# Optimization experiments

Measured on AMD Instinct MI355X. Metric: run time of the kernel, lower is better.

Reference implementation:

```python
import jax, jax.numpy as jnp
import numpy as np

B, Hs, Ws, C = 1, 48, 48, 768
NH = 12
HD = C // NH          # 64
L = Hs * Ws           # 2304
THETA = 10000.0
SCALE = HD ** -0.5
EPS = 1e-5

# relative coord index table: rel_idx[i, j] = i - j + (H - 1), as in _setup_rel_pos
_REL_IDX = jnp.asarray(np.arange(Hs)[:, None] - np.arange(Ws)[None, :] + (Hs - 1))


def _rope_cos_sin():
    """2D axial RoPE angles (compute_axial_cis): [L, HD//2] cos/sin tables."""
    nf = HD // 4
    freqs = 1.0 / (THETA ** (np.arange(0, HD, 4)[:nf].astype(np.float32) / HD))
    t = np.arange(L, dtype=np.float32)
    tx = t % Hs               # x coord cycles fastest (init_t_xy)
    ty = np.floor(t / Hs)
    ang = np.concatenate([np.outer(tx, freqs), np.outer(ty, freqs)], axis=-1)  # [L, HD//2]
    return jnp.asarray(np.cos(ang)), jnp.asarray(np.sin(ang))


def _layernorm(x, w, b):
    mu = x.mean(-1, keepdims=True)
    var = ((x - mu) ** 2).mean(-1, keepdims=True)
    return (x - mu) * jax.lax.rsqrt(var + EPS) * w + b


def _apply_rope(t, cos, sin):
    # t: [B, NH, L, HD]; view as complex pairs (even=real, odd=imag)
    tr = t.reshape(*t.shape[:-1], HD // 2, 2)
    re, im = tr[..., 0], tr[..., 1]
    out = jnp.stack([re * cos - im * sin, re * sin + im * cos], axis=-1)
    return out.reshape(t.shape)


def setup_inputs() -> dict:
    key = jax.random.key(0)
    ks = jax.random.split(key, 8)
    def rn(k, shape, std=0.02):
        return jax.random.normal(k, shape, dtype=jnp.float32) * std
    return {
        "x": jax.random.normal(ks[0], (B, Hs, Ws, C), dtype=jnp.float32),
        "ln1_w": jnp.ones((C,), jnp.float32),
        "ln1_b": jnp.zeros((C,), jnp.float32),
        "qkv_w": rn(ks[1], (3 * C, C)),
        "qkv_b": jnp.zeros((3 * C,), jnp.float32),
        "rel_pos_h": rn(ks[2], (2 * Hs - 1, HD)),
        "rel_pos_w": rn(ks[3], (2 * Ws - 1, HD)),
        "proj_w": rn(ks[4], (C, C)),
        "proj_b": jnp.zeros((C,), jnp.float32),
        "ln2_w": jnp.ones((C,), jnp.float32),
        "ln2_b": jnp.zeros((C,), jnp.float32),
        "fc1_w": rn(ks[5], (4 * C, C)),
        "fc1_b": jnp.zeros((4 * C,), jnp.float32),
        "fc2_w": rn(ks[6], (C, 4 * C)),
        "fc2_b": jnp.zeros((C,), jnp.float32),
    }


def reference(x, ln1_w, ln1_b, qkv_w, qkv_b, rel_pos_h, rel_pos_w, proj_w, proj_b,
              ln2_w, ln2_b, fc1_w, fc1_b, fc2_w, fc2_b):
    shortcut = x
    h = _layernorm(x, ln1_w, ln1_b)                         # [B,H,W,C]
    qkv = h.reshape(B, L, C) @ qkv_w.T + qkv_b              # [B,L,3C]
    qkv = qkv.reshape(B, L, 3, NH, HD).transpose(2, 0, 3, 1, 4)
    q, k, v = qkv[0], qkv[1], qkv[2]                        # [B,NH,L,HD]

    cos, sin = _rope_cos_sin()
    cos, sin = cos[None, None], sin[None, None]
    q = _apply_rope(q, cos, sin)
    k = _apply_rope(k, cos, sin)

    # Decomposed relative-position bias; math-equivalent to concat_rel_pos
    # (q' = [q*rescale, gathered-rel-vecs], k' = [k, one-hots]) followed by SDPA.
    rq = q.reshape(B, NH, Hs, Ws, HD)
    Rh = rel_pos_h[_REL_IDX]                                # [Hs, Hs(kh), HD]
    Rw = rel_pos_w[_REL_IDX]                                # [Ws, Ws(kw), HD]
    bias_h = jnp.einsum('bnhwc,hkc->bnhwk', rq, Rh)         # over key-row
    bias_w = jnp.einsum('bnhwc,wkc->bnhwk', rq, Rw)         # over key-col

    scores = jnp.einsum('bnqc,bnkc->bnqk', q, k) * SCALE    # [B,NH,L,L]
    scores = scores.reshape(B, NH, Hs, Ws, Hs, Ws) + bias_h[..., :, None] + bias_w[..., None, :]
    attn = jax.nn.softmax(scores.reshape(B, NH, L, L), axis=-1)
    out = jnp.einsum('bnqk,bnkc->bnqc', attn, v)            # [B,NH,L,HD]
    out = out.transpose(0, 2, 1, 3).reshape(B, L, C) @ proj_w.T + proj_b

    x = shortcut + out.reshape(B, Hs, Ws, C)
    h = _layernorm(x, ln2_w, ln2_b)
    h = jax.nn.gelu(h @ fc1_w.T + fc1_b, approximate=False)
    x = x + (h @ fc2_w.T + fc2_b)
    return x
```

## Files before the change

### kernel.cpp

```cpp
#include <hip/hip_runtime.h>
#include <math.h>

#define LTOK 2304
#define CDIM 768
#define NHEAD 12
#define HDIM 64
#define HS 48

typedef short s16x8 __attribute__((ext_vector_type(8)));
typedef float f32x4 __attribute__((ext_vector_type(4)));

__device__ __forceinline__ unsigned short f2b(float f) {
  __bf16 b = (__bf16)f;
  return __builtin_bit_cast(unsigned short, b);
}
__device__ __forceinline__ float b2f(unsigned short u) {
  unsigned int x = ((unsigned int)u) << 16;
  return __builtin_bit_cast(float, x);
}

__device__ __forceinline__ void gld_lds16(void* lds, const void* g) {
  __builtin_amdgcn_global_load_lds(
      (const __attribute__((address_space(1))) unsigned int*)g,
      (__attribute__((address_space(3))) unsigned int*)lds, 16, 0, 0);
}

__global__ __launch_bounds__(256) void f2b_kernel(const float* __restrict__ in,
                                                  unsigned short* __restrict__ out, int n) {
  const int i = (blockIdx.x * 256 + threadIdx.x) * 8;
  if (i + 8 > n) return;
  float4 v0 = *(const float4*)(in + i);
  float4 v1 = *(const float4*)(in + i + 4);
  alignas(16) unsigned short o[8] = {f2b(v0.x), f2b(v0.y), f2b(v0.z), f2b(v0.w),
                                     f2b(v1.x), f2b(v1.y), f2b(v1.z), f2b(v1.w)};
  *(uint4*)(out + i) = *(const uint4*)o;
}

__global__ __launch_bounds__(256) void ln_kernel(const float* __restrict__ x,
                                                 const float* __restrict__ w,
                                                 const float* __restrict__ b,
                                                 unsigned short* __restrict__ out) {
  const int row = blockIdx.x;
  const int t = threadIdx.x;
  const float* xr = x + (size_t)row * CDIM;
  float v0 = xr[t], v1 = xr[t + 256], v2 = xr[t + 512];
  float s = v0 + v1 + v2;
  float ss = v0 * v0 + v1 * v1 + v2 * v2;
#pragma unroll
  for (int off = 32; off > 0; off >>= 1) {
    s += __shfl_down(s, off, 64);
    ss += __shfl_down(ss, off, 64);
  }
  __shared__ float rs[4], rss[4];
  if ((t & 63) == 0) { rs[t >> 6] = s; rss[t >> 6] = ss; }
  __syncthreads();
  float S = rs[0] + rs[1] + rs[2] + rs[3];
  float SS = rss[0] + rss[1] + rss[2] + rss[3];
  const float inv_c = 1.0f / (float)CDIM;
  float mu = S * inv_c;
  float var = SS * inv_c - mu * mu;
  float inv = rsqrtf(var + 1e-5f);
  unsigned short* orow = out + (size_t)row * CDIM;
  orow[t]       = f2b((v0 - mu) * inv * w[t]       + b[t]);
  orow[t + 256] = f2b((v1 - mu) * inv * w[t + 256] + b[t + 256]);
  orow[t + 512] = f2b((v2 - mu) * inv * w[t + 512] + b[t + 512]);
}

template <bool GELU, bool RES, bool OUTBF>
__global__ __launch_bounds__(256) void mfma_gemm(const unsigned short* __restrict__ A,
                                                 const unsigned short* __restrict__ B,
                                                 const float* __restrict__ bias,
                                                 const float* __restrict__ res,
                                                 void* __restrict__ Cout,
                                                 int M, int N, int K) {
  __shared__ unsigned short As[128 * 32];
  __shared__ unsigned short Bs[128 * 32];
  const int t = threadIdx.x;
  const int lane = t & 63;
  const int w = t >> 6;
  const int wm = w >> 1, wn = w & 1;
  const int bm = blockIdx.y * 128, bn = blockIdx.x * 128;

  f32x4 acc[4][4] = {};

  const int c0 = 2 * w, c1 = 2 * w + 1;
  const int srow = lane >> 2;
  const int skof = (lane & 3) * 8;
  const unsigned short* Abase = A + (size_t)bm * K + skof;
  const unsigned short* Bbase = B + (size_t)bn * K + skof;
  const int lr = lane & 15, lk = (lane >> 4) * 8, lg = lane >> 4;

  for (int k0 = 0; k0 < K; k0 += 32) {
    gld_lds16(As + c0 * 512, Abase + (size_t)(c0 * 16 + srow) * K + k0);
    gld_lds16(As + c1 * 512, Abase + (size_t)(c1 * 16 + srow) * K + k0);
    gld_lds16(Bs + c0 * 512, Bbase + (size_t)(c0 * 16 + srow) * K + k0);
    gld_lds16(Bs + c1 * 512, Bbase + (size_t)(c1 * 16 + srow) * K + k0);
    __syncthreads();
    s16x8 a[4], b[4];
#pragma unroll
    for (int m = 0; m < 4; ++m)
      a[m] = *(const s16x8*)&As[(wm * 64 + m * 16 + lr) * 32 + lk];
#pragma unroll
    for (int n = 0; n < 4; ++n)
      b[n] = *(const s16x8*)&Bs[(wn * 64 + n * 16 + lr) * 32 + lk];
#pragma unroll
    for (int m = 0; m < 4; ++m)
#pragma unroll
      for (int n = 0; n < 4; ++n)
        acc[m][n] = __builtin_amdgcn_mfma_f32_16x16x32_bf16(a[m], b[n], acc[m][n], 0, 0, 0);
    __syncthreads();
  }

#pragma unroll
  for (int n = 0; n < 4; ++n) {
    const int col = bn + wn * 64 + n * 16 + lr;
    const float bc = bias[col];
#pragma unroll
    for (int m = 0; m < 4; ++m) {
#pragma unroll
      for (int j = 0; j < 4; ++j) {
        const int row = bm + wm * 64 + m * 16 + lg * 4 + j;
        float v = acc[m][n][j] + bc;
        if (GELU) v = 0.5f * v * (1.0f + erff(v * 0.70710678118654752f));
        if (RES) v += res[(size_t)row * N + col];
        if (OUTBF) ((unsigned short*)Cout)[(size_t)row * N + col] = f2b(v);
        else       ((float*)Cout)[(size_t)row * N + col] = v;
      }
    }
  }
}

__global__ __launch_bounds__(256) void rope_cs_kernel(float* __restrict__ cs,
                                                      float* __restrict__ sn) {
  const int idx = blockIdx.x * 256 + threadIdx.x;
  const int l = idx >> 5;
  const int i = idx & 31;
  const int j = i & 15;
  const float f = __expf(-(float)j * 0.57564627324851142f);
  const float coord = (i < 16) ? (float)(l % HS) : (float)(l / HS);
  const float ang = coord * f;
  cs[idx] = cosf(ang);
  sn[idx] = sinf(ang);
}

__global__ __launch_bounds__(256) void prep_kernel(const float* __restrict__ qkv,
                                                   const float* __restrict__ cs,
                                                   const float* __restrict__ sn,
                                                   unsigned short* __restrict__ Qb,
                                                   unsigned short* __restrict__ Kb,
                                                   unsigned short* __restrict__ Vb) {
  __shared__ unsigned short Vs[64 * 72];
  const int t = threadIdx.x;
  const int l0 = blockIdx.x * 64, n = blockIdx.y;
  const int r = t >> 2, c = t & 3;
  const int l = l0 + r;
  const float* base = qkv + (size_t)l * (3 * CDIM) + n * HDIM + c * 16;
#pragma unroll
  for (int pq = 0; pq < 2; ++pq) {
    const float* src = base + pq * CDIM;
    const float qs = pq ? 1.0f : 0.125f;
    alignas(16) unsigned short o[16];
#pragma unroll
    for (int i = 0; i < 4; ++i) {
      float4 v = *(const float4*)(src + i * 4);
      const int pr = c * 8 + i * 2;
      const float c0 = cs[l * 32 + pr],     s0 = sn[l * 32 + pr];
      const float c1 = cs[l * 32 + pr + 1], s1 = sn[l * 32 + pr + 1];
      o[i * 4 + 0] = f2b((v.x * c0 - v.y * s0) * qs);
      o[i * 4 + 1] = f2b((v.x * s0 + v.y * c0) * qs);
      o[i * 4 + 2] = f2b((v.z * c1 - v.w * s1) * qs);
      o[i * 4 + 3] = f2b((v.z * s1 + v.w * c1) * qs);
    }
    unsigned short* dst = (pq ? Kb : Qb) + ((size_t)n * LTOK + l) * HDIM + c * 16;
    *(uint4*)dst = *(const uint4*)o;
    *(uint4*)(dst + 8) = *(const uint4*)(o + 8);
  }
  {
    const float* vsrc = base + 2 * CDIM;
    alignas(16) unsigned short vo[16];
#pragma unroll
    for (int i = 0; i < 4; ++i) {
      float4 v = *(const float4*)(vsrc + i * 4);
      vo[i * 4 + 0] = f2b(v.x); vo[i * 4 + 1] = f2b(v.y);
      vo[i * 4 + 2] = f2b(v.z); vo[i * 4 + 3] = f2b(v.w);
    }
    *(uint4*)&Vs[r * 72 + c * 16] = *(const uint4*)vo;
    *(uint4*)&Vs[r * 72 + c * 16 + 8] = *(const uint4*)(vo + 8);
  }
  __syncthreads();
  {
    const int d = t >> 2, kc16 = (t & 3) * 16;
    alignas(16) unsigned short o[16];
#pragma unroll
    for (int i = 0; i < 16; ++i) o[i] = Vs[(kc16 + i) * 72 + d];
    const int kb = (l0 + kc16) >> 3;
    unsigned short* dst0 = Vb + ((size_t)(n * (LTOK / 8) + kb) * 64 + d) * 8;
    unsigned short* dst1 = Vb + ((size_t)(n * (LTOK / 8) + kb + 1) * 64 + d) * 8;
    *(uint4*)dst0 = *(const uint4*)o;
    *(uint4*)dst1 = *(const uint4*)(o + 8);
  }
}

__global__ __launch_bounds__(256) void attn_mfma(const unsigned short* __restrict__ Qb,
                                                 const unsigned short* __restrict__ Kb,
                                                 const unsigned short* __restrict__ Vb,
                                                 const float* __restrict__ relh,
                                                 const float* __restrict__ relw,
                                                 unsigned short* __restrict__ out) {
  __shared__ __align__(16) unsigned char smem[74752];
  unsigned short* const K_lds = (unsigned short*)(smem);
  unsigned short* const V_lds = (unsigned short*)(smem + 24576);
  unsigned short* const P_lds = (unsigned short*)(smem + 53248);
  float* const bh_t = (float*)(smem + 62464);
  unsigned short* const Q_s = (unsigned short*)(smem + 53248);

  const int t = threadIdx.x;
  const int lane = t & 63, w = t >> 6;
  const int p = lane & 15, g = lane >> 4;
  const int l0 = blockIdx.x * 64, n = blockIdx.y;

  const unsigned short* Khead = Kb + (size_t)n * LTOK * HDIM;
  const unsigned short* Vhead = Vb + (size_t)n * (LTOK / 8) * 64 * 8;

  {
    const int r = t >> 2, c = t & 3;
    const unsigned short* src = Qb + ((size_t)n * LTOK + l0 + r) * HDIM + c * 16;
    uint4 v0 = *(const uint4*)src;
    uint4 v1 = *(const uint4*)(src + 8);
    *(uint4*)&Q_s[r * 72 + c * 16] = v0;
    *(uint4*)&Q_s[r * 72 + c * 16 + 8] = v1;
  }
  __syncthreads();

  const int rowb = lane >> 3;
  const int srcc = (lane & 7) ^ rowb;
  const int kc0 = w, kc1 = w + 4, kc2 = w + 8;

  {
    gld_lds16(K_lds + kc0 * 512, Khead + (size_t)(kc0 * 8 + rowb) * HDIM + srcc * 8);
    gld_lds16(K_lds + kc1 * 512, Khead + (size_t)(kc1 * 8 + rowb) * HDIM + srcc * 8);
    gld_lds16(K_lds + kc2 * 512, Khead + (size_t)(kc2 * 8 + rowb) * HDIM + srcc * 8);
    gld_lds16(V_lds + kc0 * 512, Vhead + kc0 * 512 + lane * 8);
    gld_lds16(V_lds + kc1 * 512, Vhead + kc1 * 512 + lane * 8);
    gld_lds16(V_lds + kc2 * 512, Vhead + kc2 * 512 + lane * 8);
  }
  if (t < 128) *(uint4*)&V_lds[6144 + t * 8] = uint4{0u, 0u, 0u, 0u};
  else         *(uint4*)&V_lds[7168 + 6144 + (t - 128) * 8] = uint4{0u, 0u, 0u, 0u};

  const s16x8 qf0 = *(const s16x8*)&Q_s[(w * 16 + p) * 72 + g * 8];
  const s16x8 qf1 = *(const s16x8*)&Q_s[(w * 16 + p) * 72 + 32 + g * 8];

  const int qh_lane = (l0 + lane) / 48;
#pragma unroll
  for (int i = 0; i < 12; ++i) {
    const int kh = w + 4 * i;
    const float* rrow = relh + (size_t)(qh_lane - kh + 47) * HDIM;
    float acc = 0.f;
#pragma unroll
    for (int c8 = 0; c8 < 8; ++c8) {
      s16x8 qv = *(const s16x8*)&Q_s[lane * 72 + c8 * 8];
      float4 ra = *(const float4*)&rrow[c8 * 8];
      float4 rb = *(const float4*)&rrow[c8 * 8 + 4];
      acc += b2f((unsigned short)qv[0]) * ra.x + b2f((unsigned short)qv[1]) * ra.y +
             b2f((unsigned short)qv[2]) * ra.z + b2f((unsigned short)qv[3]) * ra.w +
             b2f((unsigned short)qv[4]) * rb.x + b2f((unsigned short)qv[5]) * rb.y +
             b2f((unsigned short)qv[6]) * rb.z + b2f((unsigned short)qv[7]) * rb.w;
    }
    bh_t[kh * 64 + lane] = acc * 8.0f;
  }

  float bwreg[12];
  {
    const int qrow = w * 16 + p;
    const int qw_lane = (l0 + qrow) % 48;
#pragma unroll
    for (int mb = 0; mb < 3; ++mb)
#pragma unroll
      for (int jj = 0; jj < 4; ++jj) {
        const int j = 16 * mb + 4 * g + jj;
        const float* rrow = relw + (size_t)(qw_lane - j + 47) * HDIM;
        float acc = 0.f;
#pragma unroll
        for (int c8 = 0; c8 < 8; ++c8) {
          s16x8 qv = *(const s16x8*)&Q_s[qrow * 72 + c8 * 8];
          float4 ra = *(const float4*)&rrow[c8 * 8];
          float4 rb = *(const float4*)&rrow[c8 * 8 + 4];
          acc += b2f((unsigned short)qv[0]) * ra.x + b2f((unsigned short)qv[1]) * ra.y +
                 b2f((unsigned short)qv[2]) * ra.z + b2f((unsigned short)qv[3]) * ra.w +
                 b2f((unsigned short)qv[4]) * rb.x + b2f((unsigned short)qv[5]) * rb.y +
                 b2f((unsigned short)qv[6]) * rb.z + b2f((unsigned short)qv[7]) * rb.w;
        }
        bwreg[mb * 4 + jj] = acc * 8.0f;
      }
  }
  __syncthreads();

  {
    uint2 z = {0u, 0u};
    *(uint2*)&P_lds[(w * 16 + p) * 72 + 48 + 4 * g] = z;
  }

  float lsum = 0.f;
  f32x4 accO[4] = {};
  const int sw0 = g ^ (p & 7);
  const int sw1 = (g + 4) ^ (p & 7);
  unsigned short* const Pw = P_lds + w * 16 * 72;

#pragma unroll 1
  for (int kt = 0; kt < 24; ++kt) {
    const int ko = (kt & 1) * 6144;
    const int vo = (kt & 1) * 7168;
    if (kt < 23) {
      const int nko = 6144 - ko, nvo = 7168 - vo;
      const int kb = (kt + 1) * 96;
      const int vb = (kt + 1) * 12;
      gld_lds16(K_lds + nko + kc0 * 512, Khead + (size_t)(kb + kc0 * 8 + rowb) * HDIM + srcc * 8);
      gld_lds16(K_lds + nko + kc1 * 512, Khead + (size_t)(kb + kc1 * 8 + rowb) * HDIM + srcc * 8);
      gld_lds16(K_lds + nko + kc2 * 512, Khead + (size_t)(kb + kc2 * 8 + rowb) * HDIM + srcc * 8);
      gld_lds16(V_lds + nvo + kc0 * 512, Vhead + (vb + kc0) * 512 + lane * 8);
      gld_lds16(V_lds + nvo + kc1 * 512, Vhead + (vb + kc1) * 512 + lane * 8);
      gld_lds16(V_lds + nvo + kc2 * 512, Vhead + (vb + kc2) * 512 + lane * 8);
    }

#pragma unroll 1
    for (int h = 0; h < 2; ++h) {
      f32x4 st[3] = {};
      __builtin_amdgcn_s_setprio(1);
#pragma unroll
      for (int mb = 0; mb < 3; ++mb) {
        const int krow = ko + (h * 48 + 16 * mb + p) * 64;
        s16x8 kf0 = *(const s16x8*)&K_lds[krow + sw0 * 8];
        s16x8 kf1 = *(const s16x8*)&K_lds[krow + sw1 * 8];
        st[mb] = __builtin_amdgcn_mfma_f32_16x16x32_bf16(kf0, qf0, st[mb], 0, 0, 0);
        st[mb] = __builtin_amdgcn_mfma_f32_16x16x32_bf16(kf1, qf1, st[mb], 0, 0, 0);
      }
      __builtin_amdgcn_s_setprio(0);

      const float bhv = bh_t[(2 * kt + h) * 64 + w * 16 + p] - 8.0f;
      float pv[12], ps = 0.f;
#pragma unroll
      for (int mb = 0; mb < 3; ++mb)
#pragma unroll
        for (int jj = 0; jj < 4; ++jj) {
          const float sv = st[mb][jj] + bhv + bwreg[mb * 4 + jj];
          pv[mb * 4 + jj] = __expf(sv);
          ps += pv[mb * 4 + jj];
        }
      lsum += ps;

#pragma unroll
      for (int mb = 0; mb < 3; ++mb) {
        unsigned int lo = (unsigned int)f2b(pv[mb * 4 + 0]) | ((unsigned int)f2b(pv[mb * 4 + 1]) << 16);
        unsigned int hi = (unsigned int)f2b(pv[mb * 4 + 2]) | ((unsigned int)f2b(pv[mb * 4 + 3]) << 16);
        uint2 val = {lo, hi};
        *(uint2*)&Pw[p * 72 + 16 * mb + 4 * g] = val;
      }

      const s16x8 pf0 = *(const s16x8*)&Pw[p * 72 + g * 8];
      const s16x8 pf1 = *(const s16x8*)&Pw[p * 72 + 32 + g * 8];
      __builtin_amdgcn_s_setprio(1);
#pragma unroll
      for (int db = 0; db < 4; ++db) {
        const int drow = 16 * db + p;
        s16x8 vf0 = *(const s16x8*)&V_lds[vo + ((6 * h + g) * 64 + drow) * 8];
        s16x8 vf1 = *(const s16x8*)&V_lds[vo + ((6 * h + 4 + g) * 64 + drow) * 8];
        accO[db] = __builtin_amdgcn_mfma_f32_16x16x32_bf16(vf0, pf0, accO[db], 0, 0, 0);
        accO[db] = __builtin_amdgcn_mfma_f32_16x16x32_bf16(vf1, pf1, accO[db], 0, 0, 0);
      }
      __builtin_amdgcn_s_setprio(0);
    }

    __syncthreads();
  }

  float ls = lsum + __shfl_xor(lsum, 16, 64);
  ls += __shfl_xor(ls, 32, 64);
  const float inv = 1.0f / ls;
  unsigned short* orow = out + (size_t)(l0 + w * 16 + p) * CDIM + n * HDIM;
#pragma unroll
  for (int db = 0; db < 4; ++db) {
    unsigned int lo = (unsigned int)f2b(accO[db][0] * inv) | ((unsigned int)f2b(accO[db][1] * inv) << 16);
    unsigned int hi = (unsigned int)f2b(accO[db][2] * inv) | ((unsigned int)f2b(accO[db][3] * inv) << 16);
    uint2 val = {lo, hi};
    *(uint2*)&orow[16 * db + 4 * g] = val;
  }
}

extern "C" void kernel_launch(void* const* d_in, const int* in_sizes, int n_in,
                              void* d_out, int out_size, void* d_ws, size_t ws_size,
                              hipStream_t stream) {
  const float* x     = (const float*)d_in[0];
  const float* ln1w  = (const float*)d_in[1];
  const float* ln1b  = (const float*)d_in[2];
  const float* qkvw  = (const float*)d_in[3];
  const float* qkvb  = (const float*)d_in[4];
  const float* relh  = (const float*)d_in[5];
  const float* relw  = (const float*)d_in[6];
  const float* projw = (const float*)d_in[7];
  const float* projb = (const float*)d_in[8];
  const float* ln2w  = (const float*)d_in[9];
  const float* ln2b  = (const float*)d_in[10];
  const float* fc1w  = (const float*)d_in[11];
  const float* fc1b  = (const float*)d_in[12];
  const float* fc2w  = (const float*)d_in[13];
  const float* fc2b  = (const float*)d_in[14];
  float* out = (float*)d_out;
  float* ws = (float*)d_ws;

  float* qkv = ws;
  float* x1  = qkv + (size_t)LTOK * 3 * CDIM;
  float* cs  = x1 + (size_t)LTOK * CDIM;
  float* sn  = cs + (size_t)LTOK * 32;
  unsigned short* h_bf    = (unsigned short*)(sn + (size_t)LTOK * 32);
  unsigned short* attn_bf = h_bf + (size_t)LTOK * CDIM;
  unsigned short* wq      = attn_bf + (size_t)LTOK * CDIM;
  unsigned short* wproj   = wq + (size_t)3 * CDIM * CDIM;
  unsigned short* wfc1    = wproj + (size_t)CDIM * CDIM;
  unsigned short* wfc2    = wfc1 + (size_t)4 * CDIM * CDIM;
  unsigned short* Qb      = (unsigned short*)x1;
  unsigned short* Kb      = Qb + (size_t)NHEAD * LTOK * HDIM;
  unsigned short* Vb      = wq;
  unsigned short* m1_bf   = (unsigned short*)qkv;

  f2b_kernel<<<(3 * CDIM * CDIM / 8 + 255) / 256, 256, 0, stream>>>(qkvw, wq, 3 * CDIM * CDIM);
  f2b_kernel<<<(CDIM * CDIM / 8 + 255) / 256, 256, 0, stream>>>(projw, wproj, CDIM * CDIM);
  f2b_kernel<<<(4 * CDIM * CDIM / 8 + 255) / 256, 256, 0, stream>>>(fc1w, wfc1, 4 * CDIM * CDIM);
  f2b_kernel<<<(4 * CDIM * CDIM / 8 + 255) / 256, 256, 0, stream>>>(fc2w, wfc2, 4 * CDIM * CDIM);

  ln_kernel<<<LTOK, 256, 0, stream>>>(x, ln1w, ln1b, h_bf);
  mfma_gemm<false, false, false><<<dim3(18, 18), 256, 0, stream>>>(
      h_bf, wq, qkvb, nullptr, qkv, LTOK, 3 * CDIM, CDIM);
  rope_cs_kernel<<<288, 256, 0, stream>>>(cs, sn);
  prep_kernel<<<dim3(36, 12), 256, 0, stream>>>(qkv, cs, sn, Qb, Kb, Vb);
  attn_mfma<<<dim3(36, 12), 256, 0, stream>>>(Qb, Kb, Vb, relh, relw, attn_bf);
  mfma_gemm<false, true, false><<<dim3(6, 18), 256, 0, stream>>>(
      attn_bf, wproj, projb, x, x1, LTOK, CDIM, CDIM);
  ln_kernel<<<LTOK, 256, 0, stream>>>(x1, ln2w, ln2b, h_bf);
  mfma_gemm<true, false, true><<<dim3(24, 18), 256, 0, stream>>>(
      h_bf, wfc1, fc1b, nullptr, m1_bf, LTOK, 4 * CDIM, CDIM);
  mfma_gemm<false, true, false><<<dim3(6, 18), 256, 0, stream>>>(
      m1_bf, wfc2, fc2b, x1, out, LTOK, CDIM, 4 * CDIM);
}
```

Measured before the change: 276.1 us.

## Split attention key tiles across two wave groups with 512-thread blocks

The attention kernel now launches 512 threads per block. The two 48-key halves of each 96-key tile, previously walked in sequence by one wave, go to separate wave groups (h = w>>2). The half-1 waves pass their partial output accumulators and row sums to the half-0 waves through shared memory at the end. The row-bias table is stored as bf16 so the larger LDS footprint still fits. This aims to double the waves resident per CU and hide MFMA and exp latency on a grid of only 432 blocks, at the cost of an extra reduction step, more LDS, and bf16 rounding of the row bias.

```diff
diff --git a/kernel.cpp b/kernel.cpp
--- a/kernel.cpp
+++ b/kernel.cpp
@@ -201,59 +201,63 @@
   }
 }
 
-__global__ __launch_bounds__(256) void attn_mfma(const unsigned short* __restrict__ Qb,
-                                                 const unsigned short* __restrict__ Kb,
-                                                 const unsigned short* __restrict__ Vb,
-                                                 const float* __restrict__ relh,
-                                                 const float* __restrict__ relw,
-                                                 unsigned short* __restrict__ out) {
-  __shared__ __align__(16) unsigned char smem[74752];
+__global__ __launch_bounds__(512, 4) void attn_mfma(const unsigned short* __restrict__ Qb,
+                                                    const unsigned short* __restrict__ Kb,
+                                                    const unsigned short* __restrict__ Vb,
+                                                    const float* __restrict__ relh,
+                                                    const float* __restrict__ relw,
+                                                    unsigned short* __restrict__ out) {
+  __shared__ __align__(16) unsigned char smem[77824];
   unsigned short* const K_lds = (unsigned short*)(smem);
   unsigned short* const V_lds = (unsigned short*)(smem + 24576);
   unsigned short* const P_lds = (unsigned short*)(smem + 53248);
-  float* const bh_t = (float*)(smem + 62464);
+  unsigned short* const bh16 = (unsigned short*)(smem + 71680);
   unsigned short* const Q_s = (unsigned short*)(smem + 53248);
+  float* const acc_sh = (float*)(smem);
+  float* const ls_sh = (float*)(smem + 16384);
 
   const int t = threadIdx.x;
   const int lane = t & 63, w = t >> 6;
+  const int wq = w & 3, h = w >> 2;
   const int p = lane & 15, g = lane >> 4;
+  const int qrow = wq * 16 + p;
   const int l0 = blockIdx.x * 64, n = blockIdx.y;
 
   const unsigned short* Khead = Kb + (size_t)n * LTOK * HDIM;
   const unsigned short* Vhead = Vb + (size_t)n * (LTOK / 8) * 64 * 8;
 
   {
-    const int r = t >> 2, c = t & 3;
-    const unsigned short* src = Qb + ((size_t)n * LTOK + l0 + r) * HDIM + c * 16;
-    uint4 v0 = *(const uint4*)src;
-    uint4 v1 = *(const uint4*)(src + 8);
-    *(uint4*)&Q_s[r * 72 + c * 16] = v0;
-    *(uint4*)&Q_s[r * 72 + c * 16 + 8] = v1;
+    const int r = t >> 3, c8 = (t & 7) * 8;
+    *(uint4*)&Q_s[r * 72 + c8] =
+        *(const uint4*)(Qb + ((size_t)n * LTOK + l0 + r) * HDIM + c8);
   }
   __syncthreads();
 
   const int rowb = lane >> 3;
   const int srcc = (lane & 7) ^ rowb;
-  const int kc0 = w, kc1 = w + 4, kc2 = w + 8;
-
-  {
-    gld_lds16(K_lds + kc0 * 512, Khead + (size_t)(kc0 * 8 + rowb) * HDIM + srcc * 8);
-    gld_lds16(K_lds + kc1 * 512, Khead + (size_t)(kc1 * 8 + rowb) * HDIM + srcc * 8);
-    gld_lds16(K_lds + kc2 * 512, Khead + (size_t)(kc2 * 8 + rowb) * HDIM + srcc * 8);
-    gld_lds16(V_lds + kc0 * 512, Vhead + kc0 * 512 + lane * 8);
-    gld_lds16(V_lds + kc1 * 512, Vhead + kc1 * 512 + lane * 8);
-    gld_lds16(V_lds + kc2 * 512, Vhead + kc2 * 512 + lane * 8);
+  const int kcA = w;
+  const int kcB = 8 + w;
+  const int vcA = w;
+  const int vcB = 8 + (w - 4);
+
+  {
+    gld_lds16(K_lds + kcA * 512, Khead + (size_t)(kcA * 8 + rowb) * HDIM + srcc * 8);
+    if (w < 4)
+      gld_lds16(K_lds + kcB * 512, Khead + (size_t)(kcB * 8 + rowb) * HDIM + srcc * 8);
+    gld_lds16(V_lds + vcA * 512, Vhead + vcA * 512 + lane * 8);
+    if (w >= 4)
+      gld_lds16(V_lds + vcB * 512, Vhead + vcB * 512 + lane * 8);
   }
   if (t < 128) *(uint4*)&V_lds[6144 + t * 8] = uint4{0u, 0u, 0u, 0u};
-  else         *(uint4*)&V_lds[7168 + 6144 + (t - 128) * 8] = uint4{0u, 0u, 0u, 0u};
-
-  const s16x8 qf0 = *(const s16x8*)&Q_s[(w * 16 + p) * 72 + g * 8];
-  const s16x8 qf1 = *(const s16x8*)&Q_s[(w * 16 + p) * 72 + 32 + g * 8];
+  else if (t < 256) *(uint4*)&V_lds[7168 + 6144 + (t - 128) * 8] = uint4{0u, 0u, 0u, 0u};
+
+  const s16x8 qf0 = *(const s16x8*)&Q_s[qrow * 72 + g * 8];
+  const s16x8 qf1 = *(const s16x8*)&Q_s[qrow * 72 + 32 + g * 8];
 
   const int qh_lane = (l0 + lane) / 48;
 #pragma unroll
-  for (int i = 0; i < 12; ++i) {
-    const int kh = w + 4 * i;
+  for (int i = 0; i < 6; ++i) {
+    const int kh = w + 8 * i;
     const float* rrow = relh + (size_t)(qh_lane - kh + 47) * HDIM;
     float acc = 0.f;
 #pragma unroll
@@ -266,12 +270,11 @@
              b2f((unsigned short)qv[4]) * rb.x + b2f((unsigned short)qv[5]) * rb.y +
              b2f((unsigned short)qv[6]) * rb.z + b2f((unsigned short)qv[7]) * rb.w;
     }
-    bh_t[kh * 64 + lane] = acc * 8.0f;
+    bh16[kh * 64 + lane] = f2b(acc * 8.0f);
   }
 
   float bwreg[12];
   {
-    const int qrow = w * 16 + p;
     const int qw_lane = (l0 + qrow) % 48;
 #pragma unroll
     for (int mb = 0; mb < 3; ++mb)
@@ -297,14 +300,14 @@
 
   {
     uint2 z = {0u, 0u};
-    *(uint2*)&P_lds[(w * 16 + p) * 72 + 48 + 4 * g] = z;
+    *(uint2*)&P_lds[w * 1152 + p * 72 + 48 + 4 * g] = z;
   }
 
   float lsum = 0.f;
   f32x4 accO[4] = {};
   const int sw0 = g ^ (p & 7);
   const int sw1 = (g + 4) ^ (p & 7);
-  unsigned short* const Pw = P_lds + w * 16 * 72;
+  unsigned short* const Pw = P_lds + w * 1152;
 
 #pragma unroll 1
   for (int kt = 0; kt < 24; ++kt) {
@@ -314,75 +317,87 @@
       const int nko = 6144 - ko, nvo = 7168 - vo;
       const int kb = (kt + 1) * 96;
       const int vb = (kt + 1) * 12;
-      gld_lds16(K_lds + nko + kc0 * 512, Khead + (size_t)(kb + kc0 * 8 + rowb) * HDIM + srcc * 8);
-      gld_lds16(K_lds + nko + kc1 * 512, Khead + (size_t)(kb + kc1 * 8 + rowb) * HDIM + srcc * 8);
-      gld_lds16(K_lds + nko + kc2 * 512, Khead + (size_t)(kb + kc2 * 8 + rowb) * HDIM + srcc * 8);
-      gld_lds16(V_lds + nvo + kc0 * 512, Vhead + (vb + kc0) * 512 + lane * 8);
-      gld_lds16(V_lds + nvo + kc1 * 512, Vhead + (vb + kc1) * 512 + lane * 8);
-      gld_lds16(V_lds + nvo + kc2 * 512, Vhead + (vb + kc2) * 512 + lane * 8);
-    }
-
-#pragma unroll 1
-    for (int h = 0; h < 2; ++h) {
-      f32x4 st[3] = {};
-      __builtin_amdgcn_s_setprio(1);
-#pragma unroll
-      for (int mb = 0; mb < 3; ++mb) {
-        const int krow = ko + (h * 48 + 16 * mb + p) * 64;
-        s16x8 kf0 = *(const s16x8*)&K_lds[krow + sw0 * 8];
-        s16x8 kf1 = *(const s16x8*)&K_lds[krow + sw1 * 8];
-        st[mb] = __builtin_amdgcn_mfma_f32_16x16x32_bf16(kf0, qf0, st[mb], 0, 0, 0);
-        st[mb] = __builtin_amdgcn_mfma_f32_16x16x32_bf16(kf1, qf1, st[mb], 0, 0, 0);
+      gld_lds16(K_lds + nko + kcA * 512, Khead + (size_t)(kb + kcA * 8 + rowb) * HDIM + srcc * 8);
+      if (w < 4)
+        gld_lds16(K_lds + nko + kcB * 512, Khead + (size_t)(kb + kcB * 8 + rowb) * HDIM + srcc * 8);
+      gld_lds16(V_lds + nvo + vcA * 512, Vhead + (vb + vcA) * 512 + lane * 8);
+      if (w >= 4)
+        gld_lds16(V_lds + nvo + vcB * 512, Vhead + (vb + vcB) * 512 + lane * 8);
+    }
+
+    f32x4 st[3] = {};
+    __builtin_amdgcn_s_setprio(1);
+#pragma unroll
+    for (int mb = 0; mb < 3; ++mb) {
+      const int krow = ko + (h * 48 + 16 * mb + p) * 64;
+      s16x8 kf0 = *(const s16x8*)&K_lds[krow + sw0 * 8];
+      s16x8 kf1 = *(const s16x8*)&K_lds[krow + sw1 * 8];
+      st[mb] = __builtin_amdgcn_mfma_f32_16x16x32_bf16(kf0, qf0, st[mb], 0, 0, 0);
+      st[mb] = __builtin_amdgcn_mfma_f32_16x16x32_bf16(kf1, qf1, st[mb], 0, 0, 0);
+    }
+    __builtin_amdgcn_s_setprio(0);
+
+    const float bhv = b2f(bh16[(2 * kt + h) * 64 + qrow]) - 8.0f;
+    float pv[12], ps = 0.f;
+#pragma unroll
+    for (int mb = 0; mb < 3; ++mb)
+#pragma unroll
+      for (int jj = 0; jj < 4; ++jj) {
+        const float sv = st[mb][jj] + bhv + bwreg[mb * 4 + jj];
+        pv[mb * 4 + jj] = __expf(sv);
+        ps += pv[mb * 4 + jj];
       }
-      __builtin_amdgcn_s_setprio(0);
-
-      const float bhv = bh_t[(2 * kt + h) * 64 + w * 16 + p] - 8.0f;
-      float pv[12], ps = 0.f;
-#pragma unroll
-      for (int mb = 0; mb < 3; ++mb)
-#pragma unroll
-        for (int jj = 0; jj < 4; ++jj) {
-          const float sv = st[mb][jj] + bhv + bwreg[mb * 4 + jj];
-          pv[mb * 4 + jj] = __expf(sv);
-          ps += pv[mb * 4 + jj];
-        }
-      lsum += ps;
-
-#pragma unroll
-      for (int mb = 0; mb < 3; ++mb) {
-        unsigned int lo = (unsigned int)f2b(pv[mb * 4 + 0]) | ((unsigned int)f2b(pv[mb * 4 + 1]) << 16);
-        unsigned int hi = (unsigned int)f2b(pv[mb * 4 + 2]) | ((unsigned int)f2b(pv[mb * 4 + 3]) << 16);
-        uint2 val = {lo, hi};
-        *(uint2*)&Pw[p * 72 + 16 * mb + 4 * g] = val;
-      }
-
-      const s16x8 pf0 = *(const s16x8*)&Pw[p * 72 + g * 8];
-      const s16x8 pf1 = *(const s16x8*)&Pw[p * 72 + 32 + g * 8];
-      __builtin_amdgcn_s_setprio(1);
-#pragma unroll
-      for (int db = 0; db < 4; ++db) {
-        const int drow = 16 * db + p;
-        s16x8 vf0 = *(const s16x8*)&V_lds[vo + ((6 * h + g) * 64 + drow) * 8];
-        s16x8 vf1 = *(const s16x8*)&V_lds[vo + ((6 * h + 4 + g) * 64 + drow) * 8];
-        accO[db] = __builtin_amdgcn_mfma_f32_16x16x32_bf16(vf0, pf0, accO[db], 0, 0, 0);
-        accO[db] = __builtin_amdgcn_mfma_f32_16x16x32_bf16(vf1, pf1, accO[db], 0, 0, 0);
-      }
-      __builtin_amdgcn_s_setprio(0);
-    }
+    lsum += ps;
+
+#pragma unroll
+    for (int mb = 0; mb < 3; ++mb) {
+      unsigned int lo = (unsigned int)f2b(pv[mb * 4 + 0]) | ((unsigned int)f2b(pv[mb * 4 + 1]) << 16);
+      unsigned int hi = (unsigned int)f2b(pv[mb * 4 + 2]) | ((unsigned int)f2b(pv[mb * 4 + 3]) << 16);
+      uint2 val = {lo, hi};
+      *(uint2*)&Pw[p * 72 + 16 * mb + 4 * g] = val;
+    }
+
+    const s16x8 pf0 = *(const s16x8*)&Pw[p * 72 + g * 8];
+    const s16x8 pf1 = *(const s16x8*)&Pw[p * 72 + 32 + g * 8];
+    __builtin_amdgcn_s_setprio(1);
+#pragma unroll
+    for (int db = 0; db < 4; ++db) {
+      const int drow = 16 * db + p;
+      s16x8 vf0 = *(const s16x8*)&V_lds[vo + ((6 * h + g) * 64 + drow) * 8];
+      s16x8 vf1 = *(const s16x8*)&V_lds[vo + ((6 * h + 4 + g) * 64 + drow) * 8];
+      accO[db] = __builtin_amdgcn_mfma_f32_16x16x32_bf16(vf0, pf0, accO[db], 0, 0, 0);
+      accO[db] = __builtin_amdgcn_mfma_f32_16x16x32_bf16(vf1, pf1, accO[db], 0, 0, 0);
+    }
+    __builtin_amdgcn_s_setprio(0);
 
     __syncthreads();
   }
 
-  float ls = lsum + __shfl_xor(lsum, 16, 64);
-  ls += __shfl_xor(ls, 32, 64);
-  const float inv = 1.0f / ls;
-  unsigned short* orow = out + (size_t)(l0 + w * 16 + p) * CDIM + n * HDIM;
-#pragma unroll
-  for (int db = 0; db < 4; ++db) {
-    unsigned int lo = (unsigned int)f2b(accO[db][0] * inv) | ((unsigned int)f2b(accO[db][1] * inv) << 16);
-    unsigned int hi = (unsigned int)f2b(accO[db][2] * inv) | ((unsigned int)f2b(accO[db][3] * inv) << 16);
-    uint2 val = {lo, hi};
-    *(uint2*)&orow[16 * db + 4 * g] = val;
+  if (h == 1) {
+    const int base = (wq * 64 + lane) * 16;
+#pragma unroll
+    for (int db = 0; db < 4; ++db)
+      *(f32x4*)&acc_sh[base + db * 4] = accO[db];
+    ls_sh[wq * 64 + lane] = lsum;
+  }
+  __syncthreads();
+  if (h == 0) {
+    const int base = (wq * 64 + lane) * 16;
+#pragma unroll
+    for (int db = 0; db < 4; ++db)
+      accO[db] += *(const f32x4*)&acc_sh[base + db * 4];
+    lsum += ls_sh[wq * 64 + lane];
+    float ls = lsum + __shfl_xor(lsum, 16, 64);
+    ls += __shfl_xor(ls, 32, 64);
+    const float inv = 1.0f / ls;
+    unsigned short* orow = out + (size_t)(l0 + qrow) * CDIM + n * HDIM;
+#pragma unroll
+    for (int db = 0; db < 4; ++db) {
+      unsigned int lo = (unsigned int)f2b(accO[db][0] * inv) | ((unsigned int)f2b(accO[db][1] * inv) << 16);
+      unsigned int hi = (unsigned int)f2b(accO[db][2] * inv) | ((unsigned int)f2b(accO[db][3] * inv) << 16);
+      uint2 val = {lo, hi};
+      *(uint2*)&orow[16 * db + 4 * g] = val;
+    }
   }
 }
 
@@ -432,7 +447,7 @@
       h_bf, wq, qkvb, nullptr, qkv, LTOK, 3 * CDIM, CDIM);
   rope_cs_kernel<<<288, 256, 0, stream>>>(cs, sn);
   prep_kernel<<<dim3(36, 12), 256, 0, stream>>>(qkv, cs, sn, Qb, Kb, Vb);
-  attn_mfma<<<dim3(36, 12), 256, 0, stream>>>(Qb, Kb, Vb, relh, relw, attn_bf);
+  attn_mfma<<<dim3(36, 12), 512, 0, stream>>>(Qb, Kb, Vb, relh, relw, attn_bf);
   mfma_gemm<false, true, false><<<dim3(6, 18), 256, 0, stream>>>(
       attn_bf, wproj, projb, x, x1, LTOK, CDIM, CDIM);
   ln_kernel<<<LTOK, 256, 0, stream>>>(x1, ln2w, ln2b, h_bf);
```

New measurement: 309.6 us. 1.12x slower.

## Merge weight conversions into one launch and use 64-row tiles for N=768 GEMMs

Applied to the files above, without the earlier changes.

Replaces four separate fp32-to-bf16 weight conversion launches with a single kernel that picks source and destination by index range. Adds a gemm64 variant with 64x128 tiles and switches the proj and fc2 GEMMs to it, doubling their grid from 108 to 216 blocks so more of the GPU's compute units have work. The smaller tiles lower per-block operand reuse, and fc2 with K=3072 now loads more total tile traffic.

```diff
diff --git a/kernel.cpp b/kernel.cpp
--- a/kernel.cpp
+++ b/kernel.cpp
@@ -25,15 +25,28 @@
       (__attribute__((address_space(3))) unsigned int*)lds, 16, 0, 0);
 }
 
-__global__ __launch_bounds__(256) void f2b_kernel(const float* __restrict__ in,
-                                                  unsigned short* __restrict__ out, int n) {
-  const int i = (blockIdx.x * 256 + threadIdx.x) * 8;
-  if (i + 8 > n) return;
-  float4 v0 = *(const float4*)(in + i);
-  float4 v1 = *(const float4*)(in + i + 4);
+__global__ __launch_bounds__(256) void f2b4_kernel(const float* __restrict__ a0,
+                                                   const float* __restrict__ a1,
+                                                   const float* __restrict__ a2,
+                                                   const float* __restrict__ a3,
+                                                   unsigned short* __restrict__ d0,
+                                                   unsigned short* __restrict__ d1,
+                                                   unsigned short* __restrict__ d2,
+                                                   unsigned short* __restrict__ d3) {
+  const int v = blockIdx.x * 256 + threadIdx.x;
+  const float* src;
+  unsigned short* dst;
+  int off;
+  if (v < 221184)      { src = a0; dst = d0; off = v; }
+  else if (v < 294912) { src = a1; dst = d1; off = v - 221184; }
+  else if (v < 589824) { src = a2; dst = d2; off = v - 294912; }
+  else                 { src = a3; dst = d3; off = v - 589824; }
+  const int i = off * 8;
+  float4 v0 = *(const float4*)(src + i);
+  float4 v1 = *(const float4*)(src + i + 4);
   alignas(16) unsigned short o[8] = {f2b(v0.x), f2b(v0.y), f2b(v0.z), f2b(v0.w),
                                      f2b(v1.x), f2b(v1.y), f2b(v1.z), f2b(v1.w)};
-  *(uint4*)(out + i) = *(const uint4*)o;
+  *(uint4*)(dst + i) = *(const uint4*)o;
 }
 
 __global__ __launch_bounds__(256) void ln_kernel(const float* __restrict__ x,
@@ -120,6 +133,68 @@
 #pragma unroll
       for (int j = 0; j < 4; ++j) {
         const int row = bm + wm * 64 + m * 16 + lg * 4 + j;
+        float v = acc[m][n][j] + bc;
+        if (GELU) v = 0.5f * v * (1.0f + erff(v * 0.70710678118654752f));
+        if (RES) v += res[(size_t)row * N + col];
+        if (OUTBF) ((unsigned short*)Cout)[(size_t)row * N + col] = f2b(v);
+        else       ((float*)Cout)[(size_t)row * N + col] = v;
+      }
+    }
+  }
+}
+
+template <bool GELU, bool RES, bool OUTBF>
+__global__ __launch_bounds__(256) void gemm64(const unsigned short* __restrict__ A,
+                                              const unsigned short* __restrict__ B,
+                                              const float* __restrict__ bias,
+                                              const float* __restrict__ res,
+                                              void* __restrict__ Cout,
+                                              int M, int N, int K) {
+  __shared__ unsigned short As[64 * 32];
+  __shared__ unsigned short Bs[128 * 32];
+  const int t = threadIdx.x;
+  const int lane = t & 63;
+  const int w = t >> 6;
+  const int wm = w >> 1, wn = w & 1;
+  const int bm = blockIdx.y * 64, bn = blockIdx.x * 128;
+
+  f32x4 acc[2][4] = {};
+
+  const int srow = lane >> 2;
+  const int skof = (lane & 3) * 8;
+  const unsigned short* Abase = A + (size_t)bm * K + skof;
+  const unsigned short* Bbase = B + (size_t)bn * K + skof;
+  const int lr = lane & 15, lk = (lane >> 4) * 8, lg = lane >> 4;
+
+  for (int k0 = 0; k0 < K; k0 += 32) {
+    gld_lds16(As + w * 512, Abase + (size_t)(w * 16 + srow) * K + k0);
+    gld_lds16(Bs + w * 512, Bbase + (size_t)(w * 16 + srow) * K + k0);
+    gld_lds16(Bs + (4 + w) * 512, Bbase + (size_t)((4 + w) * 16 + srow) * K + k0);
+    __syncthreads();
+    s16x8 a[2], b[4];
+#pragma unroll
+    for (int m = 0; m < 2; ++m)
+      a[m] = *(const s16x8*)&As[(wm * 32 + m * 16 + lr) * 32 + lk];
+#pragma unroll
+    for (int n = 0; n < 4; ++n)
+      b[n] = *(const s16x8*)&Bs[(wn * 64 + n * 16 + lr) * 32 + lk];
+#pragma unroll
+    for (int m = 0; m < 2; ++m)
+#pragma unroll
+      for (int n = 0; n < 4; ++n)
+        acc[m][n] = __builtin_amdgcn_mfma_f32_16x16x32_bf16(a[m], b[n], acc[m][n], 0, 0, 0);
+    __syncthreads();
+  }
+
+#pragma unroll
+  for (int n = 0; n < 4; ++n) {
+    const int col = bn + wn * 64 + n * 16 + lr;
+    const float bc = bias[col];
+#pragma unroll
+    for (int m = 0; m < 2; ++m) {
+#pragma unroll
+      for (int j = 0; j < 4; ++j) {
+        const int row = bm + wm * 32 + m * 16 + lg * 4 + j;
         float v = acc[m][n][j] + bc;
         if (GELU) v = 0.5f * v * (1.0f + erff(v * 0.70710678118654752f));
         if (RES) v += res[(size_t)row * N + col];
@@ -422,10 +497,7 @@
   unsigned short* Vb      = wq;
   unsigned short* m1_bf   = (unsigned short*)qkv;
 
-  f2b_kernel<<<(3 * CDIM * CDIM / 8 + 255) / 256, 256, 0, stream>>>(qkvw, wq, 3 * CDIM * CDIM);
-  f2b_kernel<<<(CDIM * CDIM / 8 + 255) / 256, 256, 0, stream>>>(projw, wproj, CDIM * CDIM);
-  f2b_kernel<<<(4 * CDIM * CDIM / 8 + 255) / 256, 256, 0, stream>>>(fc1w, wfc1, 4 * CDIM * CDIM);
-  f2b_kernel<<<(4 * CDIM * CDIM / 8 + 255) / 256, 256, 0, stream>>>(fc2w, wfc2, 4 * CDIM * CDIM);
+  f2b4_kernel<<<3456, 256, 0, stream>>>(qkvw, projw, fc1w, fc2w, wq, wproj, wfc1, wfc2);
 
   ln_kernel<<<LTOK, 256, 0, stream>>>(x, ln1w, ln1b, h_bf);
   mfma_gemm<false, false, false><<<dim3(18, 18), 256, 0, stream>>>(
@@ -433,11 +505,11 @@
   rope_cs_kernel<<<288, 256, 0, stream>>>(cs, sn);
   prep_kernel<<<dim3(36, 12), 256, 0, stream>>>(qkv, cs, sn, Qb, Kb, Vb);
   attn_mfma<<<dim3(36, 12), 256, 0, stream>>>(Qb, Kb, Vb, relh, relw, attn_bf);
-  mfma_gemm<false, true, false><<<dim3(6, 18), 256, 0, stream>>>(
+  gemm64<false, true, false><<<dim3(6, 36), 256, 0, stream>>>(
       attn_bf, wproj, projb, x, x1, LTOK, CDIM, CDIM);
   ln_kernel<<<LTOK, 256, 0, stream>>>(x1, ln2w, ln2b, h_bf);
   mfma_gemm<true, false, true><<<dim3(24, 18), 256, 0, stream>>>(
       h_bf, wfc1, fc1b, nullptr, m1_bf, LTOK, 4 * CDIM, CDIM);
-  mfma_gemm<false, true, false><<<dim3(6, 18), 256, 0, stream>>>(
+  gemm64<false, true, false><<<dim3(6, 36), 256, 0, stream>>>(
       m1_bf, wfc2, fc2b, x1, out, LTOK, CDIM, 4 * CDIM);
 }
```

New measurement: 242.1 us. 12.3% less time.
